# Performance work log

Hardware: AMD Instinct MI355X
Metric: run time of the kernel (lower is better)

Reference implementation:

```python
import jax, jax.numpy as jnp
import numpy as np

B, T, INP, HID, ACT = 64, 1000, 64, 512, 2

def setup_inputs() -> dict:
    key = jax.random.key(0)
    k1, k2, k3, k4, k5 = jax.random.split(key, 5)
    s_hh = (6.0 / (HID + HID)) ** 0.5  # xavier_uniform bounds
    s_ih = (6.0 / (INP + HID)) ** 0.5
    s_fc = (6.0 / (HID + ACT)) ** 0.5
    return {
        "inp": jax.random.normal(k1, (B, T, INP), dtype=jnp.float32),
        "hn": jax.random.normal(k2, (1, B, HID), dtype=jnp.float32),
        "W_hh": jax.random.uniform(k3, (HID, HID), jnp.float32, -s_hh, s_hh),
        "W_ih": jax.random.uniform(k4, (INP, HID), jnp.float32, -s_ih, s_ih),
        "W_fc": jax.random.uniform(k5, (HID, ACT), jnp.float32, -s_fc, s_fc),
        "b_fc": jnp.zeros((ACT,), dtype=jnp.float32),
    }

def reference(inp, hn, W_hh, W_ih, W_fc, b_fc):
    # Precompute input projections for all timesteps in one big GEMM: [B,T,H]
    inp_proj = jnp.einsum("bti,ih->bth", inp, W_ih)
    h0 = hn[0]  # [B, H]

    def step(h, x_t):
        h_next = jax.nn.sigmoid(h @ W_hh + x_t)
        return h_next, h_next

    # scan over time: xs must be time-major
    _, hs = jax.lax.scan(step, h0, jnp.swapaxes(inp_proj, 0, 1))
    rnn_out = jnp.swapaxes(hs, 0, 1)  # [B, T, H]
    hn_last = rnn_out[:, -1, :][None]  # [1, B, H]
    out = jax.nn.sigmoid(rnn_out @ W_fc + b_fc)  # [B, T, ACT]
    return (out, hn_last, rnn_out)
```

## Files before the change

### kernel.cpp

```cpp
#include <hip/hip_runtime.h>
#include <hip/hip_bf16.h>
#include <stdint.h>
#include <math.h>

#define B   64
#define T   1000
#define INP 64
#define HID 512
#define ACT 2

#define NSLICE 4
#define MROWS  2
#define NGROUP (B / MROWS)
#define NBLOCKS (NGROUP * NSLICE)
#define NLAUNCH 256
#define WORK_PER_XCD 16
#define COLS   (HID / NSLICE)
#define NWAVES 4
#define HLPAD  544

#define FAST_GUARD 256
#define SAFE_GUARD (1 << 18)

typedef __attribute__((ext_vector_type(8))) short short8;
typedef __attribute__((ext_vector_type(4))) float floatx4;
typedef __attribute__((ext_vector_type(4))) uint32_t uint32x4;

__device__ __forceinline__ uint32x4 l2_load128(const void* p) {
  uint32x4 v;
  asm volatile("global_load_dwordx4 %0, %1, off sc0\n\t"
               "s_waitcnt vmcnt(0)"
               : "=v"(v) : "v"(p) : "memory");
  return v;
}
__device__ __forceinline__ void l2_store64(uint64_t* p, uint64_t v) {
  asm volatile("global_store_dwordx2 %0, %1, off"
               :: "v"(p), "v"(v) : "memory");
}
__device__ __forceinline__ int get_xcc_id() {
  int x;
  asm volatile("s_getreg_b32 %0, hwreg(HW_REG_XCC_ID)" : "=s"(x));
  return x & 7;
}

#define CTRL_WORDS 16

__global__ __launch_bounds__(256) void init_kernel(
    const float* __restrict__ hn, uint64_t* __restrict__ h_fast,
    uint64_t* __restrict__ h_safe, uint32_t* __restrict__ ctrl) {
  if (blockIdx.x == 0 && threadIdx.x < CTRL_WORDS) ctrl[threadIdx.x] = 0;
  const int i   = blockIdx.x * 256 + threadIdx.x;
  const int g   = i >> 9;
  const int col = i & (HID - 1);
  __hip_bfloat16 b0 = __float2bfloat16(hn[(2 * g) * HID + col]);
  __hip_bfloat16 b1 = __float2bfloat16(hn[(2 * g + 1) * HID + col]);
  const uint32_t w0 = ((uint32_t)*reinterpret_cast<unsigned short*>(&b0)) << 16;
  const uint32_t w1 = ((uint32_t)*reinterpret_cast<unsigned short*>(&b1)) << 16;
  const uint64_t v  = (uint64_t)w0 | ((uint64_t)w1 << 32);
  const size_t p1 = (size_t)NGROUP * HID + i;
  h_fast[p1] = v;
  h_safe[p1] = v;
  h_fast[i] = 0x0000FFFE0000FFFEull;
  h_safe[i] = 0x0000FFFE0000FFFEull;
}

__global__ __launch_bounds__(256) void xproj_kernel(
    const float* __restrict__ inp, const float* __restrict__ W_ih,
    float* __restrict__ rnn) {
  __shared__ float xin[16 * INP];
  const int tid = threadIdx.x;
  const long r0 = (long)blockIdx.x * 16;

  const float4* inp4 = (const float4*)(inp + r0 * INP);
  ((float4*)xin)[tid] = inp4[tid];
  __syncthreads();

  const int j = tid, j2 = tid + 256;
  float acc0[16], acc1[16];
#pragma unroll
  for (int r = 0; r < 16; ++r) { acc0[r] = 0.f; acc1[r] = 0.f; }

  for (int i = 0; i < INP; ++i) {
    const float w0 = W_ih[i * HID + j];
    const float w1 = W_ih[i * HID + j2];
#pragma unroll
    for (int r = 0; r < 16; ++r) {
      const float x = xin[r * INP + i];
      acc0[r] = fmaf(x, w0, acc0[r]);
      acc1[r] = fmaf(x, w1, acc1[r]);
    }
  }
#pragma unroll
  for (int r = 0; r < 16; ++r) {
    rnn[(r0 + r) * HID + j]  = acc0[r];
    rnn[(r0 + r) * HID + j2] = acc1[r];
  }
}

__global__ __launch_bounds__(256, 1) void rnn_mfma(
    const float* __restrict__ W_hh, float* __restrict__ rnn,
    float* __restrict__ hn_out, uint64_t* __restrict__ h_fast,
    uint64_t* __restrict__ h_safe, uint32_t* __restrict__ ctrl) {
  __shared__ __align__(16) unsigned short hl[2][MROWS][HLPAD];
  __shared__ int sh_g, sh_s, sh_work, sh_mode;

  const int tid  = threadIdx.x;

  if (tid == 0) {
    uint32_t* cnt      = ctrl;
    uint32_t* claimed  = ctrl + 8;
    uint32_t* arrivals = ctrl + 9;
    uint32_t* flag     = ctrl + 10;
    const int xcc = get_xcc_id();
    const int slot = (int)__hip_atomic_fetch_add(
        &cnt[xcc], 1u, __ATOMIC_RELAXED, __HIP_MEMORY_SCOPE_AGENT);
    int work = 0, g = 0, s = 0;
    if (slot < WORK_PER_XCD) {
      g = xcc * 4 + (slot >> 2);
      s = slot & 3;
      work = 1;
      __hip_atomic_fetch_add(claimed, 1u, __ATOMIC_RELEASE,
                             __HIP_MEMORY_SCOPE_AGENT);
    }
    const int arr = (int)__hip_atomic_fetch_add(
        arrivals, 1u, __ATOMIC_ACQ_REL, __HIP_MEMORY_SCOPE_AGENT);
    if (arr == NLAUNCH - 1) {
      const uint32_t c = __hip_atomic_load(claimed, __ATOMIC_ACQUIRE,
                                           __HIP_MEMORY_SCOPE_AGENT);
      __hip_atomic_store(flag, (c == NBLOCKS) ? 2u : 1u, __ATOMIC_RELEASE,
                         __HIP_MEMORY_SCOPE_AGENT);
    }
    uint32_t f = 0; int guard = 0;
    do {
      f = __hip_atomic_load(flag, __ATOMIC_ACQUIRE, __HIP_MEMORY_SCOPE_AGENT);
    } while (f == 0 && ++guard < (1 << 20));
    if (f != 2) {
      work = (blockIdx.x < NBLOCKS);
      g = blockIdx.x & (NGROUP - 1);
      s = blockIdx.x >> 5;
    }
    sh_g = g; sh_s = s; sh_work = work; sh_mode = (f == 2);
  }
  __syncthreads();
  if (!sh_work) return;

  const int g = __builtin_amdgcn_readfirstlane(sh_g);
  const int s = __builtin_amdgcn_readfirstlane(sh_s);
  int fastmode = __builtin_amdgcn_readfirstlane(sh_mode);

  const int lane = tid & 63;
  const int w    = tid >> 6;
  const int r0   = g * MROWS;
  const int n_base = s * COLS + w * 32;

  const int lm = lane & 15;
  const int lq = lane >> 4;
  const int cca = n_base + lm;
  const int ccb = cca + 16;

  short8 bfA[16], bfB[16];
#pragma unroll
  for (int kt = 0; kt < 16; ++kt) {
    short8 fa, fb;
#pragma unroll
    for (int i = 0; i < 8; ++i) {
      const int k = kt * 32 + lq * 8 + i;
      __hip_bfloat16 ha = __float2bfloat16(W_hh[k * HID + cca]);
      __hip_bfloat16 hb = __float2bfloat16(W_hh[k * HID + ccb]);
      fa[i] = *reinterpret_cast<short*>(&ha);
      fb[i] = *reinterpret_cast<short*>(&hb);
    }
    bfA[kt] = fa;
    bfB[kt] = fb;
  }

  const int  arow   = lm & 1;
  const bool remote = (w != s);
  const bool prod   = (lq == 0);

  long roa0 = ((long)r0 * T) * HID + cca;
  long roa1 = ((long)(r0 + 1) * T) * HID + cca;
  long rob0 = roa0 + 16, rob1 = roa1 + 16;
  float xpa0 = 0.f, xpa1 = 0.f, xpb0 = 0.f, xpb1 = 0.f;
  if (prod) {
    xpa0 = rnn[roa0]; xpa1 = rnn[roa1];
    xpb0 = rnn[rob0]; xpb1 = rnn[rob1];
  }

  for (int t = 0; t < T; ++t) {
    const int p = (t + 1) & 1;

    if (t == 0 || remote) {
      const size_t idx = ((size_t)p * NGROUP + g) * HID + 2 * tid;
      const uint32_t want = (uint32_t)t & 0xFFFFu;
      uint32x4 v = {0, 0, 0, 0};
      if (fastmode) {
        int ok = 0;
        for (int it = 0; it < FAST_GUARD; ++it) {
          v = l2_load128(h_fast + idx);
          if ((((v[0] ^ want) | (v[1] ^ want) | (v[2] ^ want) |
                (v[3] ^ want)) & 0xFFFFu) == 0) { ok = 1; break; }
        }
        if (!ok) fastmode = 0;
      }
      if (!fastmode) {
        int guard = 0;
        for (;;) {
          const uint64_t a = __hip_atomic_load(h_safe + idx, __ATOMIC_RELAXED,
                                               __HIP_MEMORY_SCOPE_AGENT);
          const uint64_t b = __hip_atomic_load(h_safe + idx + 1,
                                               __ATOMIC_RELAXED,
                                               __HIP_MEMORY_SCOPE_AGENT);
          v[0] = (uint32_t)a; v[1] = (uint32_t)(a >> 32);
          v[2] = (uint32_t)b; v[3] = (uint32_t)(b >> 32);
          if ((((v[0] ^ want) | (v[1] ^ want) | (v[2] ^ want) |
                (v[3] ^ want)) & 0xFFFFu) == 0) break;
          if (++guard > SAFE_GUARD) break;
        }
      }
      *reinterpret_cast<uint32_t*>(&hl[p][0][2 * tid]) =
          (v[0] >> 16) | (v[2] & 0xFFFF0000u);
      *reinterpret_cast<uint32_t*>(&hl[p][1][2 * tid]) =
          (v[1] >> 16) | (v[3] & 0xFFFF0000u);
    }
    __syncthreads();

    float na0 = 0.f, na1 = 0.f, nb0 = 0.f, nb1 = 0.f;
    if (prod && t + 1 < T) {
      na0 = rnn[roa0 + HID]; na1 = rnn[roa1 + HID];
      nb0 = rnn[rob0 + HID]; nb1 = rnn[rob1 + HID];
    }

    floatx4 c0a = {0.f, 0.f, 0.f, 0.f}, c1a = c0a, c2a = c0a, c3a = c0a;
    floatx4 c0b = c0a, c1b = c0a, c2b = c0a, c3b = c0a;
    const unsigned short* ap = &hl[p][arow][lq * 8];
#pragma unroll
    for (int kt = 0; kt < 16; kt += 4) {
      short8 a0 = *(const short8*)(ap + (kt + 0) * 32);
      short8 a1 = *(const short8*)(ap + (kt + 1) * 32);
      short8 a2 = *(const short8*)(ap + (kt + 2) * 32);
      short8 a3 = *(const short8*)(ap + (kt + 3) * 32);
      c0a = __builtin_amdgcn_mfma_f32_16x16x32_bf16(a0, bfA[kt + 0], c0a, 0, 0, 0);
      c0b = __builtin_amdgcn_mfma_f32_16x16x32_bf16(a0, bfB[kt + 0], c0b, 0, 0, 0);
      c1a = __builtin_amdgcn_mfma_f32_16x16x32_bf16(a1, bfA[kt + 1], c1a, 0, 0, 0);
      c1b = __builtin_amdgcn_mfma_f32_16x16x32_bf16(a1, bfB[kt + 1], c1b, 0, 0, 0);
      c2a = __builtin_amdgcn_mfma_f32_16x16x32_bf16(a2, bfA[kt + 2], c2a, 0, 0, 0);
      c2b = __builtin_amdgcn_mfma_f32_16x16x32_bf16(a2, bfB[kt + 2], c2b, 0, 0, 0);
      c3a = __builtin_amdgcn_mfma_f32_16x16x32_bf16(a3, bfA[kt + 3], c3a, 0, 0, 0);
      c3b = __builtin_amdgcn_mfma_f32_16x16x32_bf16(a3, bfB[kt + 3], c3b, 0, 0, 0);
    }

    if (prod) {
      const float za0 = (c0a[0] + c1a[0]) + (c2a[0] + c3a[0]) + xpa0;
      const float za1 = (c0a[1] + c1a[1]) + (c2a[1] + c3a[1]) + xpa1;
      const float zb0 = (c0b[0] + c1b[0]) + (c2b[0] + c3b[0]) + xpb0;
      const float zb1 = (c0b[1] + c1b[1]) + (c2b[1] + c3b[1]) + xpb1;
      const float ha0 = 1.f / (1.f + __expf(-za0));
      const float ha1 = 1.f / (1.f + __expf(-za1));
      const float hb0 = 1.f / (1.f + __expf(-zb0));
      const float hb1 = 1.f / (1.f + __expf(-zb1));
      __hip_bfloat16 ba0 = __float2bfloat16(ha0);
      __hip_bfloat16 ba1 = __float2bfloat16(ha1);
      __hip_bfloat16 bb0 = __float2bfloat16(hb0);
      __hip_bfloat16 bb1 = __float2bfloat16(hb1);
      const unsigned short ua0 = *reinterpret_cast<unsigned short*>(&ba0);
      const unsigned short ua1 = *reinterpret_cast<unsigned short*>(&ba1);
      const unsigned short ub0 = *reinterpret_cast<unsigned short*>(&bb0);
      const unsigned short ub1 = *reinterpret_cast<unsigned short*>(&bb1);

      const uint32_t tag = (uint32_t)(t + 1) & 0xFFFFu;
      const uint64_t worda =
          (uint64_t)(((uint32_t)ua0 << 16) | tag) |
          ((uint64_t)(((uint32_t)ua1 << 16) | tag) << 32);
      const uint64_t wordb =
          (uint64_t)(((uint32_t)ub0 << 16) | tag) |
          ((uint64_t)(((uint32_t)ub1 << 16) | tag) << 32);
      const size_t dbase = ((size_t)(t & 1) * NGROUP + g) * HID;
      l2_store64(h_fast + dbase + cca, worda);
      l2_store64(h_fast + dbase + ccb, wordb);
      __hip_atomic_store(h_safe + dbase + cca, worda, __ATOMIC_RELAXED,
                         __HIP_MEMORY_SCOPE_AGENT);
      __hip_atomic_store(h_safe + dbase + ccb, wordb, __ATOMIC_RELAXED,
                         __HIP_MEMORY_SCOPE_AGENT);

      hl[t & 1][0][cca] = ua0;
      hl[t & 1][1][cca] = ua1;
      hl[t & 1][0][ccb] = ub0;
      hl[t & 1][1][ccb] = ub1;

      rnn[roa0] = ha0; rnn[roa1] = ha1;
      rnn[rob0] = hb0; rnn[rob1] = hb1;
      if (t == T - 1) {
        hn_out[r0 * HID + cca]       = ha0;
        hn_out[(r0 + 1) * HID + cca] = ha1;
        hn_out[r0 * HID + ccb]       = hb0;
        hn_out[(r0 + 1) * HID + ccb] = hb1;
      }
      xpa0 = na0; xpa1 = na1; xpb0 = nb0; xpb1 = nb1;
      roa0 += HID; roa1 += HID; rob0 += HID; rob1 += HID;
    }
  }
}

__global__ __launch_bounds__(256) void fc_kernel(
    const float* __restrict__ rnn, const float* __restrict__ W_fc,
    const float* __restrict__ b_fc, float* __restrict__ out) {
  const int lane = threadIdx.x & 63;
  const int wid  = threadIdx.x >> 6;
  const long row = (long)blockIdx.x * 4 + wid;

  const float4* __restrict__ hrow = (const float4*)(rnn + row * HID);
  const float4* __restrict__ Wfc4 = (const float4*)W_fc;

  float a0 = 0.f, a1 = 0.f;
#pragma unroll
  for (int u = 0; u < 2; ++u) {
    const float4 hv = hrow[lane * 2 + u];
    const int j0 = lane * 8 + u * 4;
    const float4 wA = Wfc4[(j0 >> 1)];
    const float4 wB = Wfc4[(j0 >> 1) + 1];
    a0 += hv.x * wA.x + hv.y * wA.z + hv.z * wB.x + hv.w * wB.z;
    a1 += hv.x * wA.y + hv.y * wA.w + hv.z * wB.y + hv.w * wB.w;
  }
#pragma unroll
  for (int off = 32; off > 0; off >>= 1) {
    a0 += __shfl_down(a0, off, 64);
    a1 += __shfl_down(a1, off, 64);
  }
  if (lane == 0) {
    out[row * 2 + 0] = 1.f / (1.f + __expf(-(a0 + b_fc[0])));
    out[row * 2 + 1] = 1.f / (1.f + __expf(-(a1 + b_fc[1])));
  }
}

extern "C" void kernel_launch(void* const* d_in, const int* in_sizes, int n_in,
                              void* d_out, int out_size, void* d_ws,
                              size_t ws_size, hipStream_t stream) {
  const float* inp  = (const float*)d_in[0];
  const float* hn   = (const float*)d_in[1];
  const float* W_hh = (const float*)d_in[2];
  const float* W_ih = (const float*)d_in[3];
  const float* W_fc = (const float*)d_in[4];
  const float* b_fc = (const float*)d_in[5];

  float* out    = (float*)d_out;
  float* hn_out = out + (long)B * T * ACT;
  float* rnn    = hn_out + (long)B * HID;

  uint32_t* ctrl   = (uint32_t*)d_ws;
  uint64_t* h_fast = (uint64_t*)((char*)d_ws + 256);
  const size_t HCNT = (size_t)2 * NGROUP * HID;
  uint64_t* h_safe =
      (ws_size >= 256 + 2 * HCNT * sizeof(uint64_t)) ? (h_fast + HCNT)
                                                     : h_fast;

  hipLaunchKernelGGL(init_kernel, dim3((NGROUP * HID) / 256), dim3(256), 0,
                     stream, hn, h_fast, h_safe, ctrl);
  hipLaunchKernelGGL(xproj_kernel, dim3((B * T) / 16), dim3(256), 0, stream,
                     inp, W_ih, rnn);
  hipLaunchKernelGGL(rnn_mfma, dim3(NLAUNCH), dim3(256), 0, stream,
                     W_hh, rnn, hn_out, h_fast, h_safe, ctrl);
  hipLaunchKernelGGL(fc_kernel, dim3((B * T) / 4), dim3(256), 0, stream,
                     rnn, W_fc, b_fc, out);
}
```

Measured before the change: 1.779 ms.

## Warp-specialize RNN recurrence into compute, polling, and store/prefetch waves

Blocks grow from 256 to 512 threads. Four waves only run the MFMAs, two waves poll the remote hidden-state slices (three 64-bit words per lane, with a wave-wide __all check), and two waves write rnn outputs and prefetch the next input projection through shared memory. The aim is to take global-memory latency and polling off the critical path of the compute waves. Each block also seeds its initial state from hn directly and only polls for t>0. The cost is extra shared memory and __syncthreads traffic across more waves, plus the one-time W_hh conversion still done per block.

```diff
diff --git a/kernel.cpp b/kernel.cpp
--- a/kernel.cpp
+++ b/kernel.cpp
@@ -16,23 +16,14 @@
 #define NLAUNCH 256
 #define WORK_PER_XCD 16
 #define COLS   (HID / NSLICE)
-#define NWAVES 4
 #define HLPAD  544
 
-#define FAST_GUARD 256
+#define FAST_GUARD 512
 #define SAFE_GUARD (1 << 18)
 
 typedef __attribute__((ext_vector_type(8))) short short8;
 typedef __attribute__((ext_vector_type(4))) float floatx4;
-typedef __attribute__((ext_vector_type(4))) uint32_t uint32x4;
-
-__device__ __forceinline__ uint32x4 l2_load128(const void* p) {
-  uint32x4 v;
-  asm volatile("global_load_dwordx4 %0, %1, off sc0\n\t"
-               "s_waitcnt vmcnt(0)"
-               : "=v"(v) : "v"(p) : "memory");
-  return v;
-}
+
 __device__ __forceinline__ void l2_store64(uint64_t* p, uint64_t v) {
   asm volatile("global_store_dwordx2 %0, %1, off"
                :: "v"(p), "v"(v) : "memory");
@@ -41,6 +32,9 @@
   int x;
   asm volatile("s_getreg_b32 %0, hwreg(HW_REG_XCC_ID)" : "=s"(x));
   return x & 7;
+}
+__device__ __forceinline__ int tag_ok64(uint64_t v, uint64_t want64) {
+  return ((v ^ want64) & 0x0000FFFF0000FFFFull) == 0;
 }
 
 #define CTRL_WORDS 16
@@ -97,14 +91,17 @@
   }
 }
 
-__global__ __launch_bounds__(256, 1) void rnn_mfma(
+__global__ __launch_bounds__(512, 2) void rnn_mfma(
     const float* __restrict__ W_hh, float* __restrict__ rnn,
-    float* __restrict__ hn_out, uint64_t* __restrict__ h_fast,
-    uint64_t* __restrict__ h_safe, uint32_t* __restrict__ ctrl) {
+    float* __restrict__ hn_out, const float* __restrict__ hn,
+    uint64_t* __restrict__ h_fast, uint64_t* __restrict__ h_safe,
+    uint32_t* __restrict__ ctrl) {
   __shared__ __align__(16) unsigned short hl[2][MROWS][HLPAD];
+  __shared__ float rstage[2][MROWS][COLS];
+  __shared__ float xpbuf[2][MROWS][COLS];
   __shared__ int sh_g, sh_s, sh_work, sh_mode;
 
-  const int tid  = threadIdx.x;
+  const int tid = threadIdx.x;
 
   if (tid == 0) {
     uint32_t* cnt      = ctrl;
@@ -146,159 +143,204 @@
 
   const int g = __builtin_amdgcn_readfirstlane(sh_g);
   const int s = __builtin_amdgcn_readfirstlane(sh_s);
-  int fastmode = __builtin_amdgcn_readfirstlane(sh_mode);
+  const int fast2 = __builtin_amdgcn_readfirstlane(sh_mode);
 
   const int lane = tid & 63;
   const int w    = tid >> 6;
   const int r0   = g * MROWS;
-  const int n_base = s * COLS + w * 32;
-
-  const int lm = lane & 15;
-  const int lq = lane >> 4;
-  const int cca = n_base + lm;
-  const int ccb = cca + 16;
+  const int lm   = lane & 15;
+  const int lq   = lane >> 4;
+
+  const bool compw = (w < 4);
+  const bool pollw = (w == 4 || w == 5);
+  const bool storew = (w >= 6);
+
+  {
+    __hip_bfloat16 a0 = __float2bfloat16(hn[r0 * HID + tid]);
+    __hip_bfloat16 a1 = __float2bfloat16(hn[(r0 + 1) * HID + tid]);
+    hl[1][0][tid] = *reinterpret_cast<unsigned short*>(&a0);
+    hl[1][1][tid] = *reinterpret_cast<unsigned short*>(&a1);
+    if (tid < 2 * COLS) {
+      const int row = tid >> 7, L = tid & (COLS - 1);
+      xpbuf[0][row][L] = rnn[((long)(r0 + row) * T) * HID + s * COLS + L];
+    }
+  }
 
   short8 bfA[16], bfB[16];
-#pragma unroll
-  for (int kt = 0; kt < 16; ++kt) {
-    short8 fa, fb;
-#pragma unroll
-    for (int i = 0; i < 8; ++i) {
-      const int k = kt * 32 + lq * 8 + i;
-      __hip_bfloat16 ha = __float2bfloat16(W_hh[k * HID + cca]);
-      __hip_bfloat16 hb = __float2bfloat16(W_hh[k * HID + ccb]);
-      fa[i] = *reinterpret_cast<short*>(&ha);
-      fb[i] = *reinterpret_cast<short*>(&hb);
-    }
-    bfA[kt] = fa;
-    bfB[kt] = fb;
-  }
-
-  const int  arow   = lm & 1;
-  const bool remote = (w != s);
-  const bool prod   = (lq == 0);
-
-  long roa0 = ((long)r0 * T) * HID + cca;
-  long roa1 = ((long)(r0 + 1) * T) * HID + cca;
-  long rob0 = roa0 + 16, rob1 = roa1 + 16;
-  float xpa0 = 0.f, xpa1 = 0.f, xpb0 = 0.f, xpb1 = 0.f;
-  if (prod) {
-    xpa0 = rnn[roa0]; xpa1 = rnn[roa1];
-    xpb0 = rnn[rob0]; xpb1 = rnn[rob1];
-  }
+  int cca = 0, ccb = 0;
+  if (compw) {
+    cca = s * COLS + w * 32 + lm;
+    ccb = cca + 16;
+#pragma unroll
+    for (int kt = 0; kt < 16; ++kt) {
+      short8 fa, fb;
+#pragma unroll
+      for (int i = 0; i < 8; ++i) {
+        const int k = kt * 32 + lq * 8 + i;
+        __hip_bfloat16 ha = __float2bfloat16(W_hh[k * HID + cca]);
+        __hip_bfloat16 hb = __float2bfloat16(W_hh[k * HID + ccb]);
+        fa[i] = *reinterpret_cast<short*>(&ha);
+        fb[i] = *reinterpret_cast<short*>(&hb);
+      }
+      bfA[kt] = fa;
+      bfB[kt] = fb;
+    }
+  }
+
+  int c0 = 0, c1 = 0, c2 = 0;
+  if (pollw) {
+    const int L = (w - 4) * 64 + lane;
+    const int j0 = 3 * L;
+    c0 = (j0 + 0 < s * COLS) ? (j0 + 0) : (j0 + 0 + COLS);
+    c1 = (j0 + 1 < s * COLS) ? (j0 + 1) : (j0 + 1 + COLS);
+    c2 = (j0 + 2 < s * COLS) ? (j0 + 2) : (j0 + 2 + COLS);
+  }
+  int fastmode = fast2;
+
+  const int arow = lm & 1;
+  const bool prod = (lq == 0);
 
   for (int t = 0; t < T; ++t) {
     const int p = (t + 1) & 1;
 
-    if (t == 0 || remote) {
-      const size_t idx = ((size_t)p * NGROUP + g) * HID + 2 * tid;
-      const uint32_t want = (uint32_t)t & 0xFFFFu;
-      uint32x4 v = {0, 0, 0, 0};
+    if (pollw && t > 0) {
+      const uint64_t want64 =
+          (uint64_t)(t & 0xFFFF) * 0x0000000100000001ull;
+      const size_t base = ((size_t)p * NGROUP + g) * HID;
+      const uint64_t *p0 = h_fast + base + c0, *p1 = h_fast + base + c1,
+                     *p2 = h_fast + base + c2;
+      uint64_t va = 0, vb = 0, vc = 0;
       if (fastmode) {
-        int ok = 0;
-        for (int it = 0; it < FAST_GUARD; ++it) {
-          v = l2_load128(h_fast + idx);
-          if ((((v[0] ^ want) | (v[1] ^ want) | (v[2] ^ want) |
-                (v[3] ^ want)) & 0xFFFFu) == 0) { ok = 1; break; }
+        int it = 0;
+        for (;;) {
+          asm volatile(
+              "global_load_dwordx2 %0, %3, off sc0\n\t"
+              "global_load_dwordx2 %1, %4, off sc0\n\t"
+              "global_load_dwordx2 %2, %5, off sc0\n\t"
+              "s_waitcnt vmcnt(0)"
+              : "=&v"(va), "=&v"(vb), "=&v"(vc)
+              : "v"(p0), "v"(p1), "v"(p2) : "memory");
+          const int ok = tag_ok64(va, want64) & tag_ok64(vb, want64) &
+                         tag_ok64(vc, want64);
+          if (__all(ok)) break;
+          if (++it > FAST_GUARD) { fastmode = 0; break; }
         }
-        if (!ok) fastmode = 0;
       }
       if (!fastmode) {
-        int guard = 0;
+        const uint64_t *q0 = h_safe + base + c0, *q1 = h_safe + base + c1,
+                       *q2 = h_safe + base + c2;
+        int gd = 0;
         for (;;) {
-          const uint64_t a = __hip_atomic_load(h_safe + idx, __ATOMIC_RELAXED,
-                                               __HIP_MEMORY_SCOPE_AGENT);
-          const uint64_t b = __hip_atomic_load(h_safe + idx + 1,
-                                               __ATOMIC_RELAXED,
-                                               __HIP_MEMORY_SCOPE_AGENT);
-          v[0] = (uint32_t)a; v[1] = (uint32_t)(a >> 32);
-          v[2] = (uint32_t)b; v[3] = (uint32_t)(b >> 32);
-          if ((((v[0] ^ want) | (v[1] ^ want) | (v[2] ^ want) |
-                (v[3] ^ want)) & 0xFFFFu) == 0) break;
-          if (++guard > SAFE_GUARD) break;
+          va = __hip_atomic_load(q0, __ATOMIC_RELAXED,
+                                 __HIP_MEMORY_SCOPE_AGENT);
+          vb = __hip_atomic_load(q1, __ATOMIC_RELAXED,
+                                 __HIP_MEMORY_SCOPE_AGENT);
+          vc = __hip_atomic_load(q2, __ATOMIC_RELAXED,
+                                 __HIP_MEMORY_SCOPE_AGENT);
+          const int ok = tag_ok64(va, want64) & tag_ok64(vb, want64) &
+                         tag_ok64(vc, want64);
+          if (__all(ok)) break;
+          if (++gd > SAFE_GUARD) break;
         }
       }
-      *reinterpret_cast<uint32_t*>(&hl[p][0][2 * tid]) =
-          (v[0] >> 16) | (v[2] & 0xFFFF0000u);
-      *reinterpret_cast<uint32_t*>(&hl[p][1][2 * tid]) =
-          (v[1] >> 16) | (v[3] & 0xFFFF0000u);
+      hl[p][0][c0] = (unsigned short)((uint32_t)va >> 16);
+      hl[p][1][c0] = (unsigned short)((uint32_t)(va >> 32) >> 16);
+      hl[p][0][c1] = (unsigned short)((uint32_t)vb >> 16);
+      hl[p][1][c1] = (unsigned short)((uint32_t)(vb >> 32) >> 16);
+      hl[p][0][c2] = (unsigned short)((uint32_t)vc >> 16);
+      hl[p][1][c2] = (unsigned short)((uint32_t)(vc >> 32) >> 16);
     }
     __syncthreads();
 
-    float na0 = 0.f, na1 = 0.f, nb0 = 0.f, nb1 = 0.f;
-    if (prod && t + 1 < T) {
-      na0 = rnn[roa0 + HID]; na1 = rnn[roa1 + HID];
-      nb0 = rnn[rob0 + HID]; nb1 = rnn[rob1 + HID];
-    }
-
-    floatx4 c0a = {0.f, 0.f, 0.f, 0.f}, c1a = c0a, c2a = c0a, c3a = c0a;
-    floatx4 c0b = c0a, c1b = c0a, c2b = c0a, c3b = c0a;
-    const unsigned short* ap = &hl[p][arow][lq * 8];
-#pragma unroll
-    for (int kt = 0; kt < 16; kt += 4) {
-      short8 a0 = *(const short8*)(ap + (kt + 0) * 32);
-      short8 a1 = *(const short8*)(ap + (kt + 1) * 32);
-      short8 a2 = *(const short8*)(ap + (kt + 2) * 32);
-      short8 a3 = *(const short8*)(ap + (kt + 3) * 32);
-      c0a = __builtin_amdgcn_mfma_f32_16x16x32_bf16(a0, bfA[kt + 0], c0a, 0, 0, 0);
-      c0b = __builtin_amdgcn_mfma_f32_16x16x32_bf16(a0, bfB[kt + 0], c0b, 0, 0, 0);
-      c1a = __builtin_amdgcn_mfma_f32_16x16x32_bf16(a1, bfA[kt + 1], c1a, 0, 0, 0);
-      c1b = __builtin_amdgcn_mfma_f32_16x16x32_bf16(a1, bfB[kt + 1], c1b, 0, 0, 0);
-      c2a = __builtin_amdgcn_mfma_f32_16x16x32_bf16(a2, bfA[kt + 2], c2a, 0, 0, 0);
-      c2b = __builtin_amdgcn_mfma_f32_16x16x32_bf16(a2, bfB[kt + 2], c2b, 0, 0, 0);
-      c3a = __builtin_amdgcn_mfma_f32_16x16x32_bf16(a3, bfA[kt + 3], c3a, 0, 0, 0);
-      c3b = __builtin_amdgcn_mfma_f32_16x16x32_bf16(a3, bfB[kt + 3], c3b, 0, 0, 0);
-    }
-
-    if (prod) {
-      const float za0 = (c0a[0] + c1a[0]) + (c2a[0] + c3a[0]) + xpa0;
-      const float za1 = (c0a[1] + c1a[1]) + (c2a[1] + c3a[1]) + xpa1;
-      const float zb0 = (c0b[0] + c1b[0]) + (c2b[0] + c3b[0]) + xpb0;
-      const float zb1 = (c0b[1] + c1b[1]) + (c2b[1] + c3b[1]) + xpb1;
-      const float ha0 = 1.f / (1.f + __expf(-za0));
-      const float ha1 = 1.f / (1.f + __expf(-za1));
-      const float hb0 = 1.f / (1.f + __expf(-zb0));
-      const float hb1 = 1.f / (1.f + __expf(-zb1));
-      __hip_bfloat16 ba0 = __float2bfloat16(ha0);
-      __hip_bfloat16 ba1 = __float2bfloat16(ha1);
-      __hip_bfloat16 bb0 = __float2bfloat16(hb0);
-      __hip_bfloat16 bb1 = __float2bfloat16(hb1);
-      const unsigned short ua0 = *reinterpret_cast<unsigned short*>(&ba0);
-      const unsigned short ua1 = *reinterpret_cast<unsigned short*>(&ba1);
-      const unsigned short ub0 = *reinterpret_cast<unsigned short*>(&bb0);
-      const unsigned short ub1 = *reinterpret_cast<unsigned short*>(&bb1);
-
-      const uint32_t tag = (uint32_t)(t + 1) & 0xFFFFu;
-      const uint64_t worda =
-          (uint64_t)(((uint32_t)ua0 << 16) | tag) |
-          ((uint64_t)(((uint32_t)ua1 << 16) | tag) << 32);
-      const uint64_t wordb =
-          (uint64_t)(((uint32_t)ub0 << 16) | tag) |
-          ((uint64_t)(((uint32_t)ub1 << 16) | tag) << 32);
-      const size_t dbase = ((size_t)(t & 1) * NGROUP + g) * HID;
-      l2_store64(h_fast + dbase + cca, worda);
-      l2_store64(h_fast + dbase + ccb, wordb);
-      __hip_atomic_store(h_safe + dbase + cca, worda, __ATOMIC_RELAXED,
-                         __HIP_MEMORY_SCOPE_AGENT);
-      __hip_atomic_store(h_safe + dbase + ccb, wordb, __ATOMIC_RELAXED,
-                         __HIP_MEMORY_SCOPE_AGENT);
-
-      hl[t & 1][0][cca] = ua0;
-      hl[t & 1][1][cca] = ua1;
-      hl[t & 1][0][ccb] = ub0;
-      hl[t & 1][1][ccb] = ub1;
-
-      rnn[roa0] = ha0; rnn[roa1] = ha1;
-      rnn[rob0] = hb0; rnn[rob1] = hb1;
-      if (t == T - 1) {
-        hn_out[r0 * HID + cca]       = ha0;
-        hn_out[(r0 + 1) * HID + cca] = ha1;
-        hn_out[r0 * HID + ccb]       = hb0;
-        hn_out[(r0 + 1) * HID + ccb] = hb1;
-      }
-      xpa0 = na0; xpa1 = na1; xpb0 = nb0; xpb1 = nb1;
-      roa0 += HID; roa1 += HID; rob0 += HID; rob1 += HID;
-    }
+    if (compw) {
+      floatx4 cAc[4], cBc[4];
+#pragma unroll
+      for (int j = 0; j < 4; ++j) {
+        cAc[j] = floatx4{0.f, 0.f, 0.f, 0.f};
+        cBc[j] = floatx4{0.f, 0.f, 0.f, 0.f};
+      }
+#pragma unroll
+      for (int kt = 0; kt < 16; ++kt) {
+        short8 a = *(const short8*)(&hl[p][arow][kt * 32 + lq * 8]);
+        cAc[kt & 3] = __builtin_amdgcn_mfma_f32_16x16x32_bf16(a, bfA[kt], cAc[kt & 3], 0, 0, 0);
+        cBc[kt & 3] = __builtin_amdgcn_mfma_f32_16x16x32_bf16(a, bfB[kt], cBc[kt & 3], 0, 0, 0);
+      }
+      if (prod) {
+        const int Lc = w * 32 + lm;
+        const float xa0 = xpbuf[t & 1][0][Lc];
+        const float xa1 = xpbuf[t & 1][1][Lc];
+        const float xb0 = xpbuf[t & 1][0][Lc + 16];
+        const float xb1 = xpbuf[t & 1][1][Lc + 16];
+        const float za0 = (cAc[0][0] + cAc[1][0]) + (cAc[2][0] + cAc[3][0]) + xa0;
+        const float za1 = (cAc[0][1] + cAc[1][1]) + (cAc[2][1] + cAc[3][1]) + xa1;
+        const float zb0 = (cBc[0][0] + cBc[1][0]) + (cBc[2][0] + cBc[3][0]) + xb0;
+        const float zb1 = (cBc[0][1] + cBc[1][1]) + (cBc[2][1] + cBc[3][1]) + xb1;
+        const float ha0 = 1.f / (1.f + __expf(-za0));
+        const float ha1 = 1.f / (1.f + __expf(-za1));
+        const float hb0 = 1.f / (1.f + __expf(-zb0));
+        const float hb1 = 1.f / (1.f + __expf(-zb1));
+        __hip_bfloat16 ba0 = __float2bfloat16(ha0);
+        __hip_bfloat16 ba1 = __float2bfloat16(ha1);
+        __hip_bfloat16 bb0 = __float2bfloat16(hb0);
+        __hip_bfloat16 bb1 = __float2bfloat16(hb1);
+        const unsigned short ua0 = *reinterpret_cast<unsigned short*>(&ba0);
+        const unsigned short ua1 = *reinterpret_cast<unsigned short*>(&ba1);
+        const unsigned short ub0 = *reinterpret_cast<unsigned short*>(&bb0);
+        const unsigned short ub1 = *reinterpret_cast<unsigned short*>(&bb1);
+
+        const uint32_t tag = (uint32_t)(t + 1) & 0xFFFFu;
+        const uint64_t worda =
+            (uint64_t)(((uint32_t)ua0 << 16) | tag) |
+            ((uint64_t)(((uint32_t)ua1 << 16) | tag) << 32);
+        const uint64_t wordb =
+            (uint64_t)(((uint32_t)ub0 << 16) | tag) |
+            ((uint64_t)(((uint32_t)ub1 << 16) | tag) << 32);
+        const size_t dbase = ((size_t)(t & 1) * NGROUP + g) * HID;
+        l2_store64(h_fast + dbase + cca, worda);
+        l2_store64(h_fast + dbase + ccb, wordb);
+        __hip_atomic_store(h_safe + dbase + cca, worda, __ATOMIC_RELAXED,
+                           __HIP_MEMORY_SCOPE_AGENT);
+        __hip_atomic_store(h_safe + dbase + ccb, wordb, __ATOMIC_RELAXED,
+                           __HIP_MEMORY_SCOPE_AGENT);
+
+        hl[t & 1][0][cca] = ua0;
+        hl[t & 1][1][cca] = ua1;
+        hl[t & 1][0][ccb] = ub0;
+        hl[t & 1][1][ccb] = ub1;
+        rstage[t & 1][0][Lc]      = ha0;
+        rstage[t & 1][1][Lc]      = ha1;
+        rstage[t & 1][0][Lc + 16] = hb0;
+        rstage[t & 1][1][Lc + 16] = hb1;
+        if (t == T - 1) {
+          hn_out[r0 * HID + cca]       = ha0;
+          hn_out[(r0 + 1) * HID + cca] = ha1;
+          hn_out[r0 * HID + ccb]       = hb0;
+          hn_out[(r0 + 1) * HID + ccb] = hb1;
+        }
+      }
+    } else if (storew) {
+      const int L = (w - 6) * 64 + lane;
+      const int c = s * COLS + L;
+      if (t > 0) {
+        rnn[((long)r0 * T + (t - 1)) * HID + c]       = rstage[p][0][L];
+        rnn[((long)(r0 + 1) * T + (t - 1)) * HID + c] = rstage[p][1][L];
+      }
+      if (t + 1 < T) {
+        xpbuf[(t + 1) & 1][0][L] =
+            rnn[((long)r0 * T + (t + 1)) * HID + c];
+        xpbuf[(t + 1) & 1][1][L] =
+            rnn[((long)(r0 + 1) * T + (t + 1)) * HID + c];
+      }
+    }
+  }
+
+  __syncthreads();
+  if (storew) {
+    const int L = (w - 6) * 64 + lane;
+    const int c = s * COLS + L;
+    const int pf = (T - 1) & 1;
+    rnn[((long)r0 * T + (T - 1)) * HID + c]       = rstage[pf][0][L];
+    rnn[((long)(r0 + 1) * T + (T - 1)) * HID + c] = rstage[pf][1][L];
   }
 }
 
@@ -358,8 +400,8 @@
                      stream, hn, h_fast, h_safe, ctrl);
   hipLaunchKernelGGL(xproj_kernel, dim3((B * T) / 16), dim3(256), 0, stream,
                      inp, W_ih, rnn);
-  hipLaunchKernelGGL(rnn_mfma, dim3(NLAUNCH), dim3(256), 0, stream,
-                     W_hh, rnn, hn_out, h_fast, h_safe, ctrl);
+  hipLaunchKernelGGL(rnn_mfma, dim3(NLAUNCH), dim3(512), 0, stream,
+                     W_hh, rnn, hn_out, hn, h_fast, h_safe, ctrl);
   hipLaunchKernelGGL(fc_kernel, dim3((B * T) / 4), dim3(256), 0, stream,
                      rnn, W_fc, b_fc, out);
 }
```

After: 1.968 ms. 1.11x slower.
